# Performance work log

Measured on AMD Instinct MI355X. Metric: run time of the kernel, lower is better.

The kernel has to match this reference:

```python
import jax, jax.numpy as jnp
import numpy as np

B, S, D = 16, 2048, 128

def setup_inputs() -> dict:
    key = jax.random.key(0)
    kq, kk, kv = jax.random.split(key, 3)
    return {
        "query": jax.random.normal(kq, (B, S, D), dtype=jnp.float32),
        "key": jax.random.normal(kk, (B, S, D), dtype=jnp.float32),
        "value": jax.random.normal(kv, (B, S, D), dtype=jnp.float32),
    }

def reference(query, key, value):
    # query: (B, S2, d), key: (B, S1, d), value: (B, S1, d)
    d_k = query.shape[-1]
    scale = 1.0 / jnp.sqrt(jnp.asarray(d_k, dtype=query.dtype))
    # (B, S2, S1) attention scores
    att = jnp.einsum('bqd,bkd->bqk', query, key) * scale
    att = jax.nn.softmax(att, axis=-1)
    # (B, S2, d_v)
    return jnp.einsum('bqk,bkd->bqd', att, value)
```

## Files before the change

### kernel.cpp

```cpp
#include <hip/hip_runtime.h>

#define B_N 16
#define S_LEN 2048
#define D_DIM 128
#define TK 32
#define NPH 16

typedef __attribute__((ext_vector_type(16))) float f32x16;
typedef __attribute__((ext_vector_type(8)))  short short8;
typedef __attribute__((ext_vector_type(4)))  int   i32x4;
typedef const __attribute__((address_space(1))) void* gp1;
typedef __attribute__((address_space(3))) void* sp3;
#define GLL(g, l) __builtin_amdgcn_global_load_lds((gp1)(const void*)(g), (sp3)(void*)(l), 16, 0, 0)

static __device__ __forceinline__ unsigned short f2bf(float f) {
  unsigned u = __builtin_bit_cast(unsigned, f);
  return (unsigned short)((u + 0x7fffu + ((u >> 16) & 1u)) >> 16);
}

__global__ __launch_bounds__(256)
void prep_kernel(const float* __restrict__ K, const float* __restrict__ V,
                 unsigned short* __restrict__ Kb, unsigned short* __restrict__ VT) {
  __shared__ unsigned short lds[64 * 66];
  int bx = blockIdx.x;
  int t  = threadIdx.x;
  if (bx < 1024) {
#pragma unroll
    for (int rep = 0; rep < 4; ++rep) {
      size_t i = (((size_t)rep * 1024 + bx) * 256 + t) * 4;
      float4 v = *(const float4*)(K + i);
      unsigned lo = (unsigned)f2bf(v.x) | ((unsigned)f2bf(v.y) << 16);
      unsigned hi = (unsigned)f2bf(v.z) | ((unsigned)f2bf(v.w) << 16);
      *(uint2*)(Kb + i) = make_uint2(lo, hi);
    }
  } else {
    int bi = bx - 1024;
    int b  = bi & 15;
    int st = (bi >> 4) & 31;
    int dt = bi >> 9;
    const float* Vb = V + ((size_t)b * S_LEN + st * 64) * D_DIM + dt * 64;
    unsigned short* VTb = VT + ((size_t)b * D_DIM + dt * 64) * S_LEN + st * 64;
#pragma unroll
    for (int rep = 0; rep < 4; ++rep) {
      int idx = rep * 256 + t;
      int i  = idx >> 4;
      int j4 = (idx & 15) * 4;
      float4 v = *(const float4*)(Vb + (size_t)i * D_DIM + j4);
      unsigned lo = (unsigned)f2bf(v.x) | ((unsigned)f2bf(v.y) << 16);
      unsigned hi = (unsigned)f2bf(v.z) | ((unsigned)f2bf(v.w) << 16);
      *(uint2*)&lds[i * 66 + j4] = make_uint2(lo, hi);
    }
    __syncthreads();
#pragma unroll
    for (int rep = 0; rep < 4; ++rep) {
      int idx = rep * 256 + t;
      int dd = idx >> 4;
      int s4 = (idx & 15) * 4;
      unsigned short e0 = lds[(s4 + 0) * 66 + dd];
      unsigned short e1 = lds[(s4 + 1) * 66 + dd];
      unsigned short e2 = lds[(s4 + 2) * 66 + dd];
      unsigned short e3 = lds[(s4 + 3) * 66 + dd];
      *(uint2*)(VTb + (size_t)dd * S_LEN + s4) =
          make_uint2((unsigned)e0 | ((unsigned)e1 << 16),
                     (unsigned)e2 | ((unsigned)e3 << 16));
    }
  }
}

__global__ __launch_bounds__(512, 2)
void attn_kernel(const float* __restrict__ Q, const unsigned short* __restrict__ Kb,
                 const unsigned short* __restrict__ VT, float* __restrict__ O) {
  __shared__ __align__(16) char smem[131072];

  const int tid  = threadIdx.x;
  const int wave = tid >> 6;
  const int g    = wave >> 2;
  const int w4   = wave & 3;
  const int lane = tid & 63;
  const int l32  = lane & 31;
  const int half = lane >> 5;

  const int i     = blockIdx.x;
  const int b     = (i & 7) * 2 + ((i >> 3) & 1);
  const int qtile = i >> 4;
  const int qbase = qtile * 128 + w4 * 32;

  const float* Qb = Q + (size_t)b * S_LEN * D_DIM;
  const unsigned short* Kbb = Kb + (size_t)b * S_LEN * D_DIM;
  const unsigned short* VTb = VT + (size_t)b * D_DIM * S_LEN;

  unsigned short* kb0 = (unsigned short*)smem + (size_t)g * 16384;
  unsigned short* vb0 = (unsigned short*)(smem + 65536) + (size_t)g * 16384;

#define ISSUE_PH(pp, buf)                                                          \
  {                                                                                \
    const int kb_ = g * 1024 + (pp) * 64;                                          \
    _Pragma("unroll")                                                              \
    for (int ss = 0; ss < 2; ++ss) {                                               \
      _Pragma("unroll")                                                            \
      for (int cc = 0; cc < 2; ++cc) {                                             \
        int c = w4 * 2 + cc;                                                       \
        int rl = 4 * c + (lane >> 4);                                              \
        int lbk = (lane & 15) ^ (rl & 15);                                         \
        GLL(Kbb + (size_t)(kb_ + ss * 32 + rl) * D_DIM + lbk * 8,                  \
            kb0 + (buf) * 8192 + ss * 4096 + c * 512);                             \
      }                                                                            \
    }                                                                              \
    _Pragma("unroll")                                                              \
    for (int ss = 0; ss < 2; ++ss) {                                               \
      _Pragma("unroll")                                                            \
      for (int cc = 0; cc < 2; ++cc) {                                             \
        int c = w4 * 2 + cc;                                                       \
        int dv = 16 * c + (lane >> 2);                                             \
        int lbv = (lane & 3) ^ ((dv >> 1) & 3);                                    \
        GLL(VTb + (size_t)dv * S_LEN + kb_ + ss * 32 + lbv * 8,                    \
            vb0 + (buf) * 8192 + ss * 4096 + c * 512);                             \
      }                                                                            \
    }                                                                              \
  }

#define QK_SUB(buf, ss, saccv)                                                     \
  {                                                                                \
    const unsigned short* kbc_ = kb0 + (buf) * 8192 + (ss) * 4096;                 \
    _Pragma("unroll")                                                              \
    for (int ks = 0; ks < 8; ++ks) {                                               \
      int pk = (ks * 2 + half) ^ (l32 & 15);                                       \
      short8 kf = *(const short8*)&kbc_[l32 * D_DIM + pk * 8];                     \
      saccv = __builtin_amdgcn_mfma_f32_32x32x16_bf16(kf, qa[ks], saccv, 0, 0, 0); \
    }                                                                              \
  }

#define SOFTMAX(saccv, pf0v, pf1v)                                                 \
  {                                                                                \
    float p_[16];                                                                  \
    _Pragma("unroll")                                                              \
    for (int reg = 0; reg < 16; ++reg) {                                           \
      p_[reg] = exp2f(saccv[reg] * SC);                                            \
      lsum += p_[reg];                                                             \
    }                                                                              \
    int dw_[8];                                                                    \
    _Pragma("unroll")                                                              \
    for (int i2 = 0; i2 < 8; ++i2)                                                 \
      asm("v_cvt_pk_bf16_f32 %0, %1, %2"                                           \
          : "=v"(dw_[i2]) : "v"(p_[2 * i2]), "v"(p_[2 * i2 + 1]));                 \
    asm("v_permlane32_swap_b32 %0, %1" : "+v"(dw_[0]), "+v"(dw_[2]));              \
    asm("v_permlane32_swap_b32 %0, %1" : "+v"(dw_[1]), "+v"(dw_[3]));              \
    asm("v_permlane32_swap_b32 %0, %1" : "+v"(dw_[4]), "+v"(dw_[6]));              \
    asm("v_permlane32_swap_b32 %0, %1" : "+v"(dw_[5]), "+v"(dw_[7]));              \
    i32x4 f0_ = {dw_[0], dw_[1], dw_[2], dw_[3]};                                  \
    i32x4 f1_ = {dw_[4], dw_[5], dw_[6], dw_[7]};                                  \
    pf0v = __builtin_bit_cast(short8, f0_);                                        \
    pf1v = __builtin_bit_cast(short8, f1_);                                        \
  }

#define PV_SUB(buf, ss, pf0v, pf1v)                                                \
  {                                                                                \
    const unsigned short* vbc_ = vb0 + (buf) * 8192 + (ss) * 4096;                 \
    _Pragma("unroll")                                                              \
    for (int dt = 0; dt < 4; ++dt) {                                               \
      int dv = dt * 32 + l32;                                                      \
      int pv0 = half ^ ((dv >> 1) & 3);                                            \
      short8 vf0 = *(const short8*)&vbc_[dv * TK + pv0 * 8];                       \
      oacc[dt] = __builtin_amdgcn_mfma_f32_32x32x16_bf16(pf0v, vf0, oacc[dt], 0, 0, 0); \
      int pv1 = (2 + half) ^ ((dv >> 1) & 3);                                      \
      short8 vf1 = *(const short8*)&vbc_[dv * TK + pv1 * 8];                       \
      oacc[dt] = __builtin_amdgcn_mfma_f32_32x32x16_bf16(pf1v, vf1, oacc[dt], 0, 0, 0); \
    }                                                                              \
  }

  short8 qa[8];
  {
    const float* qp = Qb + (size_t)(qbase + l32) * D_DIM + half * 8;
#pragma unroll
    for (int ks = 0; ks < 8; ++ks) {
      float4 a0 = *(const float4*)(qp + ks * 16);
      float4 a1 = *(const float4*)(qp + ks * 16 + 4);
      short8 f;
      f[0] = (short)f2bf(a0.x); f[1] = (short)f2bf(a0.y);
      f[2] = (short)f2bf(a0.z); f[3] = (short)f2bf(a0.w);
      f[4] = (short)f2bf(a1.x); f[5] = (short)f2bf(a1.y);
      f[6] = (short)f2bf(a1.z); f[7] = (short)f2bf(a1.w);
      qa[ks] = f;
    }
  }

  ISSUE_PH(0, 0)
  ISSUE_PH(1, 1)

  const f32x16 zf16 = {0.f,0.f,0.f,0.f,0.f,0.f,0.f,0.f,0.f,0.f,0.f,0.f,0.f,0.f,0.f,0.f};
  f32x16 oacc[4];
  float lsum = 0.f;
#pragma unroll
  for (int dt = 0; dt < 4; ++dt) oacc[dt] = zf16;

  const float SC = 0.08838834764831845f * 1.4426950408889634f;

  for (int t = 0; t < NPH; ++t) {
    if (t + 1 < NPH) {
      asm volatile("s_waitcnt vmcnt(8)" ::: "memory");
    } else {
      asm volatile("s_waitcnt vmcnt(0)" ::: "memory");
    }
    __builtin_amdgcn_s_barrier();

    const int cb = t & 1;

    f32x16 sacc0 = zf16, sacc1 = zf16;
    short8 pf00, pf01, pf10, pf11;

    QK_SUB(cb, 0, sacc0)
    QK_SUB(cb, 1, sacc1)
    SOFTMAX(sacc0, pf00, pf01)
    PV_SUB(cb, 0, pf00, pf01)
    SOFTMAX(sacc1, pf10, pf11)
    PV_SUB(cb, 1, pf10, pf11)

    __builtin_amdgcn_s_barrier();
    if (t + 2 < NPH) ISSUE_PH(t + 2, cb)
  }
#undef ISSUE_PH
#undef QK_SUB
#undef SOFTMAX
#undef PV_SUB

  lsum += __shfl_xor(lsum, 32);

  __syncthreads();
  float* mo  = (float*)(smem + w4 * 16640);
  float* ml1 = (float*)(smem + w4 * 16640 + 16384);
  float* ml0 = ml1 + 32;
  if (g == 1) {
#pragma unroll
    for (int reg = 0; reg < 16; ++reg) {
      int row = (reg & 3) + 8 * (reg >> 2) + 4 * half;
#pragma unroll
      for (int dt = 0; dt < 4; ++dt)
        mo[row * 128 + dt * 32 + l32] = oacc[dt][reg];
    }
    if (half == 0) ml1[l32] = lsum;
  } else {
    if (half == 0) ml0[l32] = lsum;
  }
  __syncthreads();
  if (g == 0) {
    float* Ob = O + (size_t)b * S_LEN * D_DIM;
#pragma unroll
    for (int reg = 0; reg < 16; ++reg) {
      int row = (reg & 3) + 8 * (reg >> 2) + 4 * half;
      float linv = 1.f / (ml0[row] + ml1[row]);
#pragma unroll
      for (int dt = 0; dt < 4; ++dt)
        Ob[(size_t)(qbase + row) * D_DIM + dt * 32 + l32] =
            (oacc[dt][reg] + mo[row * 128 + dt * 32 + l32]) * linv;
    }
  }
}

extern "C" void kernel_launch(void* const* d_in, const int* in_sizes, int n_in,
                              void* d_out, int out_size, void* d_ws, size_t ws_size,
                              hipStream_t stream) {
  const float* Q = (const float*)d_in[0];
  const float* K = (const float*)d_in[1];
  const float* V = (const float*)d_in[2];
  float* O = (float*)d_out;
  unsigned short* Kb = (unsigned short*)d_ws;
  unsigned short* VT = Kb + (size_t)B_N * S_LEN * D_DIM;
  prep_kernel<<<dim3(1024 + 1024), dim3(256), 0, stream>>>(K, V, Kb, VT);
  attn_kernel<<<dim3(256), dim3(512), 0, stream>>>(Q, Kb, VT, O);
}
```

Before: 139.1 us.

## Pre-swizzle K/V into MFMA fragment layout and load directly to registers

The prep kernel now writes K and V in bf16 already arranged as per-lane MFMA operand fragments, so the attention kernel loads them straight from global memory into registers instead of staging through LDS with global_load_lds and barriers. The attention kernel shrinks to 128-thread blocks (2 waves splitting the key range) over 32 query rows, launching 1024 blocks, with K double-buffered in registers. This removes LDS traffic and block-wide barriers. In exchange each wave re-reads K/V from global/L2 with no sharing across query waves, raising memory traffic, and register pressure goes up.

```diff
diff --git a/kernel.cpp b/kernel.cpp
--- a/kernel.cpp
+++ b/kernel.cpp
@@ -3,15 +3,11 @@
 #define B_N 16
 #define S_LEN 2048
 #define D_DIM 128
-#define TK 32
-#define NPH 16
+#define NTH 32
 
 typedef __attribute__((ext_vector_type(16))) float f32x16;
 typedef __attribute__((ext_vector_type(8)))  short short8;
 typedef __attribute__((ext_vector_type(4)))  int   i32x4;
-typedef const __attribute__((address_space(1))) void* gp1;
-typedef __attribute__((address_space(3))) void* sp3;
-#define GLL(g, l) __builtin_amdgcn_global_load_lds((gp1)(const void*)(g), (sp3)(void*)(l), 16, 0, 0)
 
 static __device__ __forceinline__ unsigned short f2bf(float f) {
   unsigned u = __builtin_bit_cast(unsigned, f);
@@ -20,116 +16,122 @@
 
 __global__ __launch_bounds__(256)
 void prep_kernel(const float* __restrict__ K, const float* __restrict__ V,
-                 unsigned short* __restrict__ Kb, unsigned short* __restrict__ VT) {
-  __shared__ unsigned short lds[64 * 66];
-  int bx = blockIdx.x;
-  int t  = threadIdx.x;
-  if (bx < 1024) {
-#pragma unroll
-    for (int rep = 0; rep < 4; ++rep) {
-      size_t i = (((size_t)rep * 1024 + bx) * 256 + t) * 4;
-      float4 v = *(const float4*)(K + i);
-      unsigned lo = (unsigned)f2bf(v.x) | ((unsigned)f2bf(v.y) << 16);
-      unsigned hi = (unsigned)f2bf(v.z) | ((unsigned)f2bf(v.w) << 16);
-      *(uint2*)(Kb + i) = make_uint2(lo, hi);
-    }
-  } else {
-    int bi = bx - 1024;
-    int b  = bi & 15;
-    int st = (bi >> 4) & 31;
-    int dt = bi >> 9;
-    const float* Vb = V + ((size_t)b * S_LEN + st * 64) * D_DIM + dt * 64;
-    unsigned short* VTb = VT + ((size_t)b * D_DIM + dt * 64) * S_LEN + st * 64;
-#pragma unroll
-    for (int rep = 0; rep < 4; ++rep) {
-      int idx = rep * 256 + t;
-      int i  = idx >> 4;
-      int j4 = (idx & 15) * 4;
-      float4 v = *(const float4*)(Vb + (size_t)i * D_DIM + j4);
-      unsigned lo = (unsigned)f2bf(v.x) | ((unsigned)f2bf(v.y) << 16);
-      unsigned hi = (unsigned)f2bf(v.z) | ((unsigned)f2bf(v.w) << 16);
-      *(uint2*)&lds[i * 66 + j4] = make_uint2(lo, hi);
-    }
-    __syncthreads();
-#pragma unroll
-    for (int rep = 0; rep < 4; ++rep) {
-      int idx = rep * 256 + t;
-      int dd = idx >> 4;
-      int s4 = (idx & 15) * 4;
-      unsigned short e0 = lds[(s4 + 0) * 66 + dd];
-      unsigned short e1 = lds[(s4 + 1) * 66 + dd];
-      unsigned short e2 = lds[(s4 + 2) * 66 + dd];
-      unsigned short e3 = lds[(s4 + 3) * 66 + dd];
-      *(uint2*)(VTb + (size_t)dd * S_LEN + s4) =
-          make_uint2((unsigned)e0 | ((unsigned)e1 << 16),
-                     (unsigned)e2 | ((unsigned)e3 << 16));
-    }
-  }
-}
-
-__global__ __launch_bounds__(512, 2)
-void attn_kernel(const float* __restrict__ Q, const unsigned short* __restrict__ Kb,
-                 const unsigned short* __restrict__ VT, float* __restrict__ O) {
-  __shared__ __align__(16) char smem[131072];
+                 unsigned short* __restrict__ Kf, unsigned short* __restrict__ Vf) {
+  __shared__ unsigned short lds[32 * 132];
+  const int bx = blockIdx.x;
+  const int b  = bx >> 6;
+  const int T  = bx & 63;
+  const int t  = threadIdx.x;
+
+  const float* Kb = K + ((size_t)b * S_LEN + T * 32) * D_DIM;
+  const float* Vb = V + ((size_t)b * S_LEN + T * 32) * D_DIM;
+  unsigned short* Kfb = Kf + ((size_t)(b * 64 + T) * 8) * 512;
+  unsigned short* Vfb = Vf + ((size_t)(b * 64 + T) * 8) * 512;
+
+#pragma unroll
+  for (int rep = 0; rep < 2; ++rep) {
+    int u    = rep * 256 + t;
+    int ks   = u >> 6;
+    int lane = u & 63;
+    const float* src = Kb + (size_t)(lane & 31) * D_DIM + ks * 16 + (lane >> 5) * 8;
+    float4 a0 = *(const float4*)(src);
+    float4 a1 = *(const float4*)(src + 4);
+    unsigned w0 = (unsigned)f2bf(a0.x) | ((unsigned)f2bf(a0.y) << 16);
+    unsigned w1 = (unsigned)f2bf(a0.z) | ((unsigned)f2bf(a0.w) << 16);
+    unsigned w2 = (unsigned)f2bf(a1.x) | ((unsigned)f2bf(a1.y) << 16);
+    unsigned w3 = (unsigned)f2bf(a1.z) | ((unsigned)f2bf(a1.w) << 16);
+    *(uint4*)(Kfb + (size_t)ks * 512 + lane * 8) = make_uint4(w0, w1, w2, w3);
+  }
+
+#pragma unroll
+  for (int rep = 0; rep < 2; ++rep) {
+    int id  = rep * 256 + t;
+    int row = id >> 4;
+    int c8  = (id & 15) * 8;
+    float4 a0 = *(const float4*)(Vb + (size_t)row * D_DIM + c8);
+    float4 a1 = *(const float4*)(Vb + (size_t)row * D_DIM + c8 + 4);
+    unsigned short* d = &lds[row * 132 + c8];
+    d[0] = f2bf(a0.x); d[1] = f2bf(a0.y); d[2] = f2bf(a0.z); d[3] = f2bf(a0.w);
+    d[4] = f2bf(a1.x); d[5] = f2bf(a1.y); d[6] = f2bf(a1.z); d[7] = f2bf(a1.w);
+  }
+  __syncthreads();
+
+#pragma unroll
+  for (int rep = 0; rep < 2; ++rep) {
+    int u    = rep * 256 + t;
+    int f    = u >> 6;
+    int lane = u & 63;
+    int ks2  = f >> 2;
+    int dt   = f & 3;
+    int col  = dt * 32 + (lane & 31);
+    int rbase = ks2 * 16 + (lane >> 5) * 8;
+    unsigned w[4];
+#pragma unroll
+    for (int jj = 0; jj < 4; ++jj) {
+      unsigned short e0 = lds[(rbase + 2 * jj) * 132 + col];
+      unsigned short e1 = lds[(rbase + 2 * jj + 1) * 132 + col];
+      w[jj] = (unsigned)e0 | ((unsigned)e1 << 16);
+    }
+    *(uint4*)(Vfb + (size_t)f * 512 + lane * 8) = make_uint4(w[0], w[1], w[2], w[3]);
+  }
+}
+
+__global__ __launch_bounds__(128, 2)
+void attn_kernel(const float* __restrict__ Q, const unsigned short* __restrict__ Kf,
+                 const unsigned short* __restrict__ Vf, float* __restrict__ O) {
+  __shared__ __align__(16) float smem[4160];
 
   const int tid  = threadIdx.x;
-  const int wave = tid >> 6;
-  const int g    = wave >> 2;
-  const int w4   = wave & 3;
+  const int g    = tid >> 6;
   const int lane = tid & 63;
   const int l32  = lane & 31;
   const int half = lane >> 5;
 
   const int i     = blockIdx.x;
   const int b     = (i & 7) * 2 + ((i >> 3) & 1);
-  const int qtile = i >> 4;
-  const int qbase = qtile * 128 + w4 * 32;
+  const int qt    = i >> 4;
+  const int qbase = qt * 32;
 
   const float* Qb = Q + (size_t)b * S_LEN * D_DIM;
-  const unsigned short* Kbb = Kb + (size_t)b * S_LEN * D_DIM;
-  const unsigned short* VTb = VT + (size_t)b * D_DIM * S_LEN;
-
-  unsigned short* kb0 = (unsigned short*)smem + (size_t)g * 16384;
-  unsigned short* vb0 = (unsigned short*)(smem + 65536) + (size_t)g * 16384;
-
-#define ISSUE_PH(pp, buf)                                                          \
-  {                                                                                \
-    const int kb_ = g * 1024 + (pp) * 64;                                          \
-    _Pragma("unroll")                                                              \
-    for (int ss = 0; ss < 2; ++ss) {                                               \
-      _Pragma("unroll")                                                            \
-      for (int cc = 0; cc < 2; ++cc) {                                             \
-        int c = w4 * 2 + cc;                                                       \
-        int rl = 4 * c + (lane >> 4);                                              \
-        int lbk = (lane & 15) ^ (rl & 15);                                         \
-        GLL(Kbb + (size_t)(kb_ + ss * 32 + rl) * D_DIM + lbk * 8,                  \
-            kb0 + (buf) * 8192 + ss * 4096 + c * 512);                             \
-      }                                                                            \
-    }                                                                              \
-    _Pragma("unroll")                                                              \
-    for (int ss = 0; ss < 2; ++ss) {                                               \
-      _Pragma("unroll")                                                            \
-      for (int cc = 0; cc < 2; ++cc) {                                             \
-        int c = w4 * 2 + cc;                                                       \
-        int dv = 16 * c + (lane >> 2);                                             \
-        int lbv = (lane & 3) ^ ((dv >> 1) & 3);                                    \
-        GLL(VTb + (size_t)dv * S_LEN + kb_ + ss * 32 + lbv * 8,                    \
-            vb0 + (buf) * 8192 + ss * 4096 + c * 512);                             \
-      }                                                                            \
-    }                                                                              \
-  }
-
-#define QK_SUB(buf, ss, saccv)                                                     \
-  {                                                                                \
-    const unsigned short* kbc_ = kb0 + (buf) * 8192 + (ss) * 4096;                 \
-    _Pragma("unroll")                                                              \
-    for (int ks = 0; ks < 8; ++ks) {                                               \
-      int pk = (ks * 2 + half) ^ (l32 & 15);                                       \
-      short8 kf = *(const short8*)&kbc_[l32 * D_DIM + pk * 8];                     \
-      saccv = __builtin_amdgcn_mfma_f32_32x32x16_bf16(kf, qa[ks], saccv, 0, 0, 0); \
-    }                                                                              \
-  }
-
+  const unsigned short* Kfb = Kf + ((size_t)(b * 64 + g * 32) * 8) * 512 + lane * 8;
+  const unsigned short* Vfb = Vf + ((size_t)(b * 64 + g * 32) * 8) * 512 + lane * 8;
+
+  short8 qa[8];
+  {
+    const float* qp = Qb + (size_t)(qbase + l32) * D_DIM + half * 8;
+#pragma unroll
+    for (int ks = 0; ks < 8; ++ks) {
+      float4 a0 = *(const float4*)(qp + ks * 16);
+      float4 a1 = *(const float4*)(qp + ks * 16 + 4);
+      short8 f;
+      f[0] = (short)f2bf(a0.x); f[1] = (short)f2bf(a0.y);
+      f[2] = (short)f2bf(a0.z); f[3] = (short)f2bf(a0.w);
+      f[4] = (short)f2bf(a1.x); f[5] = (short)f2bf(a1.y);
+      f[6] = (short)f2bf(a1.z); f[7] = (short)f2bf(a1.w);
+      qa[ks] = f;
+    }
+  }
+
+  const f32x16 zf16 = {0.f,0.f,0.f,0.f,0.f,0.f,0.f,0.f,0.f,0.f,0.f,0.f,0.f,0.f,0.f,0.f};
+  f32x16 oacc[4];
+  float lsum = 0.f;
+#pragma unroll
+  for (int dt = 0; dt < 4; ++dt) oacc[dt] = zf16;
+
+  const float SC = 0.08838834764831845f * 1.4426950408889634f;
+
+#define LOAD_K(dst, tt)                                                            \
+  _Pragma("unroll")                                                                \
+  for (int ks = 0; ks < 8; ++ks)                                                   \
+    dst[ks] = *(const short8*)(Kfb + (((size_t)(tt) * 8 + ks) << 9));
+#define LOAD_V(dst, tt)                                                            \
+  _Pragma("unroll")                                                                \
+  for (int f = 0; f < 8; ++f)                                                      \
+    dst[f] = *(const short8*)(Vfb + (((size_t)(tt) * 8 + f) << 9));
+#define QK(kreg, saccv)                                                            \
+  _Pragma("unroll")                                                                \
+  for (int ks = 0; ks < 8; ++ks)                                                   \
+    saccv = __builtin_amdgcn_mfma_f32_32x32x16_bf16(kreg[ks], qa[ks], saccv, 0, 0, 0);
 #define SOFTMAX(saccv, pf0v, pf1v)                                                 \
   {                                                                                \
     float p_[16];                                                                  \
@@ -152,83 +154,50 @@
     pf0v = __builtin_bit_cast(short8, f0_);                                        \
     pf1v = __builtin_bit_cast(short8, f1_);                                        \
   }
-
-#define PV_SUB(buf, ss, pf0v, pf1v)                                                \
-  {                                                                                \
-    const unsigned short* vbc_ = vb0 + (buf) * 8192 + (ss) * 4096;                 \
-    _Pragma("unroll")                                                              \
-    for (int dt = 0; dt < 4; ++dt) {                                               \
-      int dv = dt * 32 + l32;                                                      \
-      int pv0 = half ^ ((dv >> 1) & 3);                                            \
-      short8 vf0 = *(const short8*)&vbc_[dv * TK + pv0 * 8];                       \
-      oacc[dt] = __builtin_amdgcn_mfma_f32_32x32x16_bf16(pf0v, vf0, oacc[dt], 0, 0, 0); \
-      int pv1 = (2 + half) ^ ((dv >> 1) & 3);                                      \
-      short8 vf1 = *(const short8*)&vbc_[dv * TK + pv1 * 8];                       \
-      oacc[dt] = __builtin_amdgcn_mfma_f32_32x32x16_bf16(pf1v, vf1, oacc[dt], 0, 0, 0); \
-    }                                                                              \
-  }
-
-  short8 qa[8];
-  {
-    const float* qp = Qb + (size_t)(qbase + l32) * D_DIM + half * 8;
-#pragma unroll
-    for (int ks = 0; ks < 8; ++ks) {
-      float4 a0 = *(const float4*)(qp + ks * 16);
-      float4 a1 = *(const float4*)(qp + ks * 16 + 4);
-      short8 f;
-      f[0] = (short)f2bf(a0.x); f[1] = (short)f2bf(a0.y);
-      f[2] = (short)f2bf(a0.z); f[3] = (short)f2bf(a0.w);
-      f[4] = (short)f2bf(a1.x); f[5] = (short)f2bf(a1.y);
-      f[6] = (short)f2bf(a1.z); f[7] = (short)f2bf(a1.w);
-      qa[ks] = f;
-    }
-  }
-
-  ISSUE_PH(0, 0)
-  ISSUE_PH(1, 1)
-
-  const f32x16 zf16 = {0.f,0.f,0.f,0.f,0.f,0.f,0.f,0.f,0.f,0.f,0.f,0.f,0.f,0.f,0.f,0.f};
-  f32x16 oacc[4];
-  float lsum = 0.f;
-#pragma unroll
-  for (int dt = 0; dt < 4; ++dt) oacc[dt] = zf16;
-
-  const float SC = 0.08838834764831845f * 1.4426950408889634f;
-
-  for (int t = 0; t < NPH; ++t) {
-    if (t + 1 < NPH) {
-      asm volatile("s_waitcnt vmcnt(8)" ::: "memory");
-    } else {
-      asm volatile("s_waitcnt vmcnt(0)" ::: "memory");
-    }
-    __builtin_amdgcn_s_barrier();
-
-    const int cb = t & 1;
-
-    f32x16 sacc0 = zf16, sacc1 = zf16;
-    short8 pf00, pf01, pf10, pf11;
-
-    QK_SUB(cb, 0, sacc0)
-    QK_SUB(cb, 1, sacc1)
-    SOFTMAX(sacc0, pf00, pf01)
-    PV_SUB(cb, 0, pf00, pf01)
-    SOFTMAX(sacc1, pf10, pf11)
-    PV_SUB(cb, 1, pf10, pf11)
-
-    __builtin_amdgcn_s_barrier();
-    if (t + 2 < NPH) ISSUE_PH(t + 2, cb)
-  }
-#undef ISSUE_PH
-#undef QK_SUB
+#define PV(vreg, pf0v, pf1v)                                                       \
+  _Pragma("unroll")                                                                \
+  for (int dt = 0; dt < 4; ++dt) {                                                 \
+    oacc[dt] = __builtin_amdgcn_mfma_f32_32x32x16_bf16(pf0v, vreg[dt],     oacc[dt], 0, 0, 0); \
+    oacc[dt] = __builtin_amdgcn_mfma_f32_32x32x16_bf16(pf1v, vreg[4 + dt], oacc[dt], 0, 0, 0); \
+  }
+
+  short8 kA[8], kB[8];
+  LOAD_K(kA, 0)
+
+  for (int t = 0; t < NTH; t += 2) {
+    {
+      short8 vr[8];
+      LOAD_V(vr, t)
+      LOAD_K(kB, t + 1)
+      f32x16 sacc = zf16;
+      QK(kA, sacc)
+      short8 pf0, pf1;
+      SOFTMAX(sacc, pf0, pf1)
+      PV(vr, pf0, pf1)
+    }
+    {
+      short8 vr[8];
+      LOAD_V(vr, t + 1)
+      if (t + 2 < NTH) LOAD_K(kA, t + 2)
+      f32x16 sacc = zf16;
+      QK(kB, sacc)
+      short8 pf0, pf1;
+      SOFTMAX(sacc, pf0, pf1)
+      PV(vr, pf0, pf1)
+    }
+  }
+#undef LOAD_K
+#undef LOAD_V
+#undef QK
 #undef SOFTMAX
-#undef PV_SUB
+#undef PV
 
   lsum += __shfl_xor(lsum, 32);
 
   __syncthreads();
-  float* mo  = (float*)(smem + w4 * 16640);
-  float* ml1 = (float*)(smem + w4 * 16640 + 16384);
-  float* ml0 = ml1 + 32;
+  float* mo  = smem;
+  float* ml1 = smem + 4096;
+  float* ml0 = smem + 4128;
   if (g == 1) {
 #pragma unroll
     for (int reg = 0; reg < 16; ++reg) {
@@ -263,8 +232,8 @@
   const float* K = (const float*)d_in[1];
   const float* V = (const float*)d_in[2];
   float* O = (float*)d_out;
-  unsigned short* Kb = (unsigned short*)d_ws;
-  unsigned short* VT = Kb + (size_t)B_N * S_LEN * D_DIM;
-  prep_kernel<<<dim3(1024 + 1024), dim3(256), 0, stream>>>(K, V, Kb, VT);
-  attn_kernel<<<dim3(256), dim3(512), 0, stream>>>(Q, Kb, VT, O);
-}
+  unsigned short* Kf = (unsigned short*)d_ws;
+  unsigned short* Vf = Kf + (size_t)B_N * S_LEN * D_DIM;
+  prep_kernel<<<dim3(1024), dim3(256), 0, stream>>>(K, V, Kf, Vf);
+  attn_kernel<<<dim3(1024), dim3(128), 0, stream>>>(Q, Kf, Vf, O);
+}
```

Result: slower. 142.1 us (+2.1%).
